# Kernel optimization log

Measured on AMD Instinct MI355X. Metric: run time of the kernel, lower is better.

Reference implementation:

```python
import jax, jax.numpy as jnp
import numpy as np

B, N, DIN, DOUT, CHEB_K, EMBED = 64, 2048, 64, 64, 3, 16


def setup_inputs() -> dict:
    key = jax.random.key(0)
    k0, k1, k2, k3 = jax.random.split(key, 4)
    return {
        "x": jax.random.normal(k0, (B, N, DIN), dtype=jnp.float32),
        "node_embeddings": jax.random.normal(k1, (N, EMBED), dtype=jnp.float32),
        "weights_pool": jax.random.normal(k2, (EMBED, CHEB_K, DIN, DOUT), dtype=jnp.float32) * 0.02,
        "bias_pool": jax.random.normal(k3, (EMBED, DOUT), dtype=jnp.float32) * 0.02,
    }


def reference(x, node_embeddings, weights_pool, bias_pool):
    # x: (B, N, dim_in); node_embeddings: (N, embed_dim)
    n = node_embeddings.shape[0]
    # adaptive adjacency: softmax(relu(E E^T)) row-wise
    supports = jax.nn.softmax(jax.nn.relu(node_embeddings @ node_embeddings.T), axis=1)
    # Chebyshev polynomial basis: T0=I, T1=S, Tk = 2 S T_{k-1} - T_{k-2}
    tk = [jnp.eye(n, dtype=x.dtype), supports]
    for _ in range(2, CHEB_K):
        tk.append(2.0 * supports @ tk[-1] - tk[-2])
    S = jnp.stack(tk, axis=0)  # (K, N, N)
    # per-node weights/bias generated from embeddings
    weights = jnp.einsum('nd,dkio->nkio', node_embeddings, weights_pool)  # (N,K,din,dout)
    bias = node_embeddings @ bias_pool  # (N, dout)
    # graph conv: aggregate over neighbors for each Chebyshev order
    x_g = jnp.einsum('knm,bmc->bnkc', S, x)  # (B, N, K, din)
    out = jnp.einsum('bnki,nkio->bno', x_g, weights) + bias  # (B, N, dout)
    return out
```

## Files before the change

### kernel.cpp

```cpp
#include <hip/hip_runtime.h>
#include <hip/hip_bf16.h>

typedef unsigned short u16;
typedef short short8 __attribute__((ext_vector_type(8)));
typedef short short4v __attribute__((ext_vector_type(4)));
typedef float floatx4 __attribute__((ext_vector_type(4)));

#define NNODES 2048
#define BATCH  64
#define DIN    64
#define DOUT   64
#define EMB    16

__device__ __forceinline__ u16 f2bf(float f) {
  union { float f; unsigned u; } v; v.f = f;
  unsigned r = v.u + 0x7fffu + ((v.u >> 16) & 1u);
  return (u16)(r >> 16);
}

__device__ __forceinline__ void gload_lds16(const void* g, void* l) {
  __builtin_amdgcn_global_load_lds(
      (const __attribute__((address_space(1))) void*)g,
      (__attribute__((address_space(3))) void*)l, 16, 0, 0);
}

__global__ __launch_bounds__(256) void wgen_k(const float* __restrict__ E,
                                              const float* __restrict__ pool,
                                              u16* __restrict__ W) {
  int t = threadIdx.x;
  int ec = blockIdx.x % 48, nc = blockIdx.x / 48;
  int e = ec * 256 + t;
  int n0 = nc * 64;
  float pv[16];
#pragma unroll
  for (int d = 0; d < 16; d++) {
    float p = pool[(size_t)d * 12288 + e];
    if (e < 4096) p -= pool[(size_t)d * 12288 + 8192 + e];
    if (e >= 8192) p += p;
    pv[d] = p;
  }
  const float* er = E + (size_t)n0 * EMB;
#pragma unroll 4
  for (int nn = 0; nn < 64; nn++) {
    float acc = 0.0f;
#pragma unroll
    for (int d = 0; d < 16; d++) acc = fmaf(er[nn * EMB + d], pv[d], acc);
    W[(size_t)(n0 + nn) * 12288 + e] = f2bf(acc);
  }
}

__global__ __launch_bounds__(256) void prologue(const float* __restrict__ E,
                                                const float* __restrict__ x,
                                                u16* __restrict__ Sb,
                                                u16* __restrict__ xtt) {
  int bid = blockIdx.x;
  int t = threadIdx.x;

  if (bid < 2048) {
    int n = bid;
    const float4* ep = (const float4*)(E + (size_t)n * EMB);
    float4 e0 = ep[0], e1 = ep[1], e2 = ep[2], e3 = ep[3];
    float lg[8];
    float mx = 0.0f;
#pragma unroll
    for (int j = 0; j < 8; j++) {
      int m = t + j * 256;
      const float4* mp = (const float4*)(E + (size_t)m * EMB);
      float4 a = mp[0], b = mp[1], c = mp[2], d = mp[3];
      float dot = e0.x * a.x + e0.y * a.y + e0.z * a.z + e0.w * a.w
                + e1.x * b.x + e1.y * b.y + e1.z * b.z + e1.w * b.w
                + e2.x * c.x + e2.y * c.y + e2.z * c.z + e2.w * c.w
                + e3.x * d.x + e3.y * d.y + e3.z * d.z + e3.w * d.w;
      dot = fmaxf(dot, 0.0f);
      lg[j] = dot;
      mx = fmaxf(mx, dot);
    }
    __shared__ float smax[4], ssum[4];
#pragma unroll
    for (int off = 32; off > 0; off >>= 1) mx = fmaxf(mx, __shfl_xor(mx, off, 64));
    if ((t & 63) == 0) smax[t >> 6] = mx;
    __syncthreads();
    mx = fmaxf(fmaxf(smax[0], smax[1]), fmaxf(smax[2], smax[3]));
    float sum = 0.0f;
#pragma unroll
    for (int j = 0; j < 8; j++) {
      float e = __expf(lg[j] - mx);
      lg[j] = e;
      sum += e;
    }
#pragma unroll
    for (int off = 32; off > 0; off >>= 1) sum += __shfl_xor(sum, off, 64);
    if ((t & 63) == 0) ssum[t >> 6] = sum;
    __syncthreads();
    sum = ssum[0] + ssum[1] + ssum[2] + ssum[3];
    float inv = 1.0f / sum;
#pragma unroll
    for (int j = 0; j < 8; j++)
      Sb[(size_t)n * NNODES + t + j * 256] = f2bf(lg[j] * inv);

  } else {
    __shared__ float tile[64][69];
    int u = bid - 2048;
    int b = u >> 5;
    int m0 = (u & 31) * 64;
    int r = t >> 2, cs = (t & 3) * 16;
    const float* xp = x + ((size_t)b * NNODES + m0 + r) * DIN + cs;
    float4 v0 = ((const float4*)xp)[0];
    float4 v1 = ((const float4*)xp)[1];
    float4 v2 = ((const float4*)xp)[2];
    float4 v3 = ((const float4*)xp)[3];
    *(float4*)&tile[r][cs]      = v0;
    *(float4*)&tile[r][cs + 4]  = v1;
    *(float4*)&tile[r][cs + 8]  = v2;
    *(float4*)&tile[r][cs + 12] = v3;
    __syncthreads();
    int c = t >> 2, ms = (t & 3) * 16;
    short8 o0, o1;
#pragma unroll
    for (int j = 0; j < 8; j++) o0[j] = (short)f2bf(tile[ms + j][c]);
#pragma unroll
    for (int j = 0; j < 8; j++) o1[j] = (short)f2bf(tile[ms + 8 + j][c]);
    u16* op = xtt + ((size_t)b * 64 + c) * NNODES + m0 + ms;
    *(short8*)op = o0;
    *(short8*)(op + 8) = o1;
  }
}

#define GK 2048
#define GN 4096
#define NT 32
#define BUFU 24576

#define GEMM_PREAMBLE                                                          \
  __shared__ u16 smem[3 * BUFU];                                               \
  int t = threadIdx.x, lane = t & 63, wave = t >> 6;                           \
  int lin = blockIdx.y * gridDim.x + blockIdx.x;                               \
  int nwg = gridDim.x * gridDim.y;                                             \
  int sw = (lin & 7) * (nwg >> 3) + (lin >> 3);                                \
  int bx = sw & 31, by = sw >> 5;                                              \
  int m0 = by * 256, n0 = bx * 128;                                            \
  const u16* pg[6];                                                            \
  int lof[6];                                                                  \
  _Pragma("unroll") for (int j = 0; j < 4; j++) {                              \
    int c = t + 512 * j;                                                       \
    int row = c >> 3;                                                          \
    int gs = (c & 7) ^ (row & 7);                                              \
    pg[j] = A + (size_t)(m0 + row) * GK + gs * 8;                              \
    lof[j] = c * 8;                                                            \
  }                                                                            \
  _Pragma("unroll") for (int j = 0; j < 2; j++) {                              \
    int c = t + 512 * j;                                                       \
    int row = c >> 3;                                                          \
    int gs = (c & 7) ^ (row & 7);                                              \
    pg[4 + j] = Bt + (size_t)(n0 + row) * GK + gs * 8;                         \
    lof[4 + j] = 16384 + c * 8;                                                \
  }                                                                            \
  auto stage = [&](int b, int kt) {                                            \
    _Pragma("unroll") for (int j = 0; j < 6; j++)                              \
        gload_lds16(pg[j] + kt, &smem[b * BUFU + lof[j]]);                     \
  };                                                                           \
  int wr = wave >> 1, wc = wave & 1;                                           \
  int lr = lane & 15, lg = lane >> 4;                                          \
  floatx4 acc[4][4];                                                           \
  _Pragma("unroll") for (int mi = 0; mi < 4; mi++)                             \
      _Pragma("unroll") for (int ni = 0; ni < 4; ni++)                         \
          acc[mi][ni] = (floatx4)0.0f;                                         \
  int aoff[2][4], boff[2][4];                                                  \
  _Pragma("unroll") for (int s = 0; s < 2; s++) {                              \
    _Pragma("unroll") for (int mi = 0; mi < 4; mi++) {                         \
      int row = wr * 64 + mi * 16 + lr;                                        \
      int slot = s * 4 + lg;                                                   \
      aoff[s][mi] = row * 64 + (slot ^ (row & 7)) * 8;                         \
    }                                                                          \
    _Pragma("unroll") for (int ni = 0; ni < 4; ni++) {                         \
      int row = wc * 64 + ni * 16 + lr;                                        \
      int slot = s * 4 + lg;                                                   \
      boff[s][ni] = 16384 + row * 64 + (slot ^ (row & 7)) * 8;                 \
    }                                                                          \
  }                                                                            \
  auto compute = [&](int b) {                                                  \
    const u16* base = &smem[b * BUFU];                                         \
    short8 af[2][4], bf[2][4];                                                 \
    _Pragma("unroll") for (int s = 0; s < 2; s++) {                            \
      _Pragma("unroll") for (int mi = 0; mi < 4; mi++)                         \
          af[s][mi] = *(const short8*)(base + aoff[s][mi]);                    \
      _Pragma("unroll") for (int ni = 0; ni < 4; ni++)                         \
          bf[s][ni] = *(const short8*)(base + boff[s][ni]);                    \
    }                                                                          \
    _Pragma("unroll") for (int s = 0; s < 2; s++)                              \
        _Pragma("unroll") for (int mi = 0; mi < 4; mi++)                       \
            _Pragma("unroll") for (int ni = 0; ni < 4; ni++)                   \
                acc[mi][ni] = __builtin_amdgcn_mfma_f32_16x16x32_bf16(         \
                    af[s][mi], bf[s][ni], acc[mi][ni], 0, 0, 0);               \
  };                                                                           \
  stage(0, 0);                                                                 \
  stage(1, 64);                                                                \
  for (int tt = 0; tt < NT - 2; ++tt) {                                        \
    asm volatile("s_waitcnt vmcnt(6)" ::: "memory");                           \
    __builtin_amdgcn_s_barrier();                                              \
    stage((tt + 2) % 3, (tt + 2) * 64);                                        \
    compute(tt % 3);                                                           \
  }                                                                            \
  asm volatile("s_waitcnt vmcnt(6)" ::: "memory");                             \
  __builtin_amdgcn_s_barrier();                                                \
  compute((NT - 2) % 3);                                                       \
  asm volatile("s_waitcnt vmcnt(0)" ::: "memory");                             \
  __builtin_amdgcn_s_barrier();                                                \
  compute((NT - 1) % 3);                                                       \
  _Pragma("unroll") for (int mi = 0; mi < 4; mi++)                             \
      _Pragma("unroll") for (int ni = 0; ni < 4; ni++) {                       \
    int row = m0 + wr * 64 + mi * 16 + lg * 4;                                 \
    int col = n0 + wc * 64 + ni * 16 + lr;                                     \
    _Pragma("unroll") for (int r = 0; r < 4; r++)                              \
        C[(size_t)(row + r) * GN + col] = f2bf(acc[mi][ni][r]);                \
  }

__global__ __launch_bounds__(512) void gemm_plain(const u16* __restrict__ A,
                                                  const u16* __restrict__ Bt,
                                                  u16* __restrict__ C) {
  GEMM_PREAMBLE
}

__global__ __launch_bounds__(512) void gemm_tr(const u16* __restrict__ A,
                                               const u16* __restrict__ Bt,
                                               u16* __restrict__ C,
                                               u16* __restrict__ Ct) {
  GEMM_PREAMBLE
  __syncthreads();
  u16* scr = smem + wave * 4608;
#pragma unroll
  for (int mi = 0; mi < 4; mi++)
#pragma unroll
    for (int ni = 0; ni < 4; ni++) {
      int ncol = ni * 16 + lr;
      int chunk = mi * 2 + (lg >> 1);
      int off = ncol * 72 + chunk * 8 + (lg & 1) * 4;
      short4v sv;
#pragma unroll
      for (int r = 0; r < 4; r++) sv[r] = (short)f2bf(acc[mi][ni][r]);
      *(short4v*)&scr[off] = sv;
    }
  int c = lane;
  u16* op = Ct + (size_t)(n0 + wc * 64 + c) * GK + m0 + wr * 64;
#pragma unroll
  for (int jj = 0; jj < 8; jj++) {
    short8 v = *(const short8*)&scr[c * 72 + jj * 8];
    *(short8*)(op + jj * 8) = v;
  }
}

__global__ __launch_bounds__(256) void final_k(const float* __restrict__ x,
                                               const float* __restrict__ E,
                                               const float* __restrict__ bpool,
                                               const u16* __restrict__ xg1,
                                               const u16* __restrict__ xg2,
                                               const u16* __restrict__ W,
                                               float* __restrict__ out) {
  __shared__ u16 Xs[3][64][72];
  __shared__ u16 Ws[64 * 200];
  __shared__ float bias_s[64];
  int n = blockIdx.x, t = threadIdx.x;

  {
    int b = t >> 2, i0 = (t & 3) * 16;
    const float* xp = x + ((size_t)b * NNODES + n) * DIN + i0;
    float4 v0 = ((const float4*)xp)[0];
    float4 v1 = ((const float4*)xp)[1];
    float4 v2 = ((const float4*)xp)[2];
    float4 v3 = ((const float4*)xp)[3];
    u16* d = &Xs[0][b][i0];
    d[0] = f2bf(v0.x); d[1] = f2bf(v0.y); d[2] = f2bf(v0.z); d[3] = f2bf(v0.w);
    d[4] = f2bf(v1.x); d[5] = f2bf(v1.y); d[6] = f2bf(v1.z); d[7] = f2bf(v1.w);
    d[8] = f2bf(v2.x); d[9] = f2bf(v2.y); d[10] = f2bf(v2.z); d[11] = f2bf(v2.w);
    d[12] = f2bf(v3.x); d[13] = f2bf(v3.y); d[14] = f2bf(v3.z); d[15] = f2bf(v3.w);
  }
  for (int idx = t; idx < 512; idx += 256) {
    short8 v1 = *(const short8*)(xg1 + (size_t)n * 4096 + idx * 8);
    *(short8*)&Xs[1][idx >> 3][(idx & 7) * 8] = v1;
    short8 v2 = *(const short8*)(xg2 + (size_t)n * 4096 + idx * 8);
    *(short8*)&Xs[2][idx >> 3][(idx & 7) * 8] = v2;
  }
  for (int idx = t; idx < 1536; idx += 256) {
    short8 v = *(const short8*)(W + (size_t)n * 12288 + idx * 8);
    int kk = idx >> 3;
    int oo = (idx & 7) * 8;
    int c8 = kk >> 3, k7 = kk & 7;
#pragma unroll
    for (int j = 0; j < 8; j++) {
      int o = oo + j;
      Ws[o * 200 + ((c8 ^ (o >> 3)) << 3) + k7] = (u16)v[j];
    }
  }
  if (t < 64) {
    float acc = 0.0f;
#pragma unroll
    for (int d = 0; d < 16; d++)
      acc = fmaf(E[(size_t)n * EMB + d], bpool[d * 64 + t], acc);
    bias_s[t] = acc;
  }
  __syncthreads();

  int lane = t & 63, wave = t >> 6;
  int lr = lane & 15, lg = lane >> 4;
  int wb = wave * 16;
  floatx4 acc[4];
#pragma unroll
  for (int ot = 0; ot < 4; ot++) acc[ot] = (floatx4)0.0f;

#pragma unroll
  for (int ks = 0; ks < 6; ks++) {
    int kk = ks * 32 + lg * 8;
    int c8 = ks * 4 + lg;
    short8 a = *(const short8*)&Xs[kk >> 6][wb + lr][kk & 63];
#pragma unroll
    for (int ot = 0; ot < 4; ot++) {
      int o = ot * 16 + lr;
      short8 bb = *(const short8*)&Ws[o * 200 + ((c8 ^ (o >> 3)) << 3)];
      acc[ot] = __builtin_amdgcn_mfma_f32_16x16x32_bf16(a, bb, acc[ot], 0, 0, 0);
    }
  }
#pragma unroll
  for (int ot = 0; ot < 4; ot++) {
    int o = ot * 16 + lr;
    float bs = bias_s[o];
#pragma unroll
    for (int r = 0; r < 4; r++) {
      int b = wb + lg * 4 + r;
      out[((size_t)b * NNODES + n) * DOUT + o] = acc[ot][r] + bs;
    }
  }
}

extern "C" void kernel_launch(void* const* d_in, const int* in_sizes, int n_in,
                              void* d_out, int out_size, void* d_ws, size_t ws_size,
                              hipStream_t stream) {
  const float* x     = (const float*)d_in[0];
  const float* E     = (const float*)d_in[1];
  const float* pool  = (const float*)d_in[2];
  const float* bpool = (const float*)d_in[3];
  float* out = (float*)d_out;

  char* ws = (char*)d_ws;
  u16* Sb   = (u16*)(ws);
  u16* xtt  = (u16*)(ws + 8388608);
  u16* xg1  = (u16*)(ws + 25165824);
  u16* xg1t = (u16*)(ws + 41943040);
  u16* xg2  = (u16*)(ws + 58720256);
  u16* Wall = (u16*)(ws + 75497472);

  prologue<<<4096, 256, 0, stream>>>(E, x, Sb, xtt);
  wgen_k<<<1536, 256, 0, stream>>>(E, pool, Wall);
  gemm_tr<<<dim3(32, 8), 512, 0, stream>>>(Sb, xtt, xg1, xg1t);
  gemm_plain<<<dim3(32, 8), 512, 0, stream>>>(Sb, xg1t, xg2);
  final_k<<<NNODES, 256, 0, stream>>>(x, E, bpool, xg1, xg2, Wall, out);
}
```

Before: 157.3 us.

## Fuse per-node weight generation into first GEMM as extra producer waves

Removes the separate weight-generation kernel and runs it inside gemm_tr as four extra waves per block (768 threads). Those waves compute three outputs each per embedding row and issue barriers to stay in step with the GEMM waves' barrier sequence. The aim is to hide the large bf16 weight write behind the compute-bound GEMM and save one launch. The cost is a larger launch bound, which may limit registers and occupancy for the GEMM waves, and the barrier counts must match exactly or the kernel breaks.

Result: slower. 163.3 us (+3.8%).

```diff
diff --git a/kernel.cpp b/kernel.cpp
--- a/kernel.cpp
+++ b/kernel.cpp
@@ -5,6 +5,7 @@
 typedef short short8 __attribute__((ext_vector_type(8)));
 typedef short short4v __attribute__((ext_vector_type(4)));
 typedef float floatx4 __attribute__((ext_vector_type(4)));
+typedef float float16v __attribute__((ext_vector_type(16)));
 
 #define NNODES 2048
 #define BATCH  64
@@ -22,31 +23,6 @@
   __builtin_amdgcn_global_load_lds(
       (const __attribute__((address_space(1))) void*)g,
       (__attribute__((address_space(3))) void*)l, 16, 0, 0);
-}
-
-__global__ __launch_bounds__(256) void wgen_k(const float* __restrict__ E,
-                                              const float* __restrict__ pool,
-                                              u16* __restrict__ W) {
-  int t = threadIdx.x;
-  int ec = blockIdx.x % 48, nc = blockIdx.x / 48;
-  int e = ec * 256 + t;
-  int n0 = nc * 64;
-  float pv[16];
-#pragma unroll
-  for (int d = 0; d < 16; d++) {
-    float p = pool[(size_t)d * 12288 + e];
-    if (e < 4096) p -= pool[(size_t)d * 12288 + 8192 + e];
-    if (e >= 8192) p += p;
-    pv[d] = p;
-  }
-  const float* er = E + (size_t)n0 * EMB;
-#pragma unroll 4
-  for (int nn = 0; nn < 64; nn++) {
-    float acc = 0.0f;
-#pragma unroll
-    for (int d = 0; d < 16; d++) acc = fmaf(er[nn * EMB + d], pv[d], acc);
-    W[(size_t)(n0 + nn) * 12288 + e] = f2bf(acc);
-  }
 }
 
 __global__ __launch_bounds__(256) void prologue(const float* __restrict__ E,
@@ -135,8 +111,7 @@
   __shared__ u16 smem[3 * BUFU];                                               \
   int t = threadIdx.x, lane = t & 63, wave = t >> 6;                           \
   int lin = blockIdx.y * gridDim.x + blockIdx.x;                               \
-  int nwg = gridDim.x * gridDim.y;                                             \
-  int sw = (lin & 7) * (nwg >> 3) + (lin >> 3);                                \
+  int sw = (lin & 7) * 32 + (lin >> 3);                     \
   int bx = sw & 31, by = sw >> 5;                                              \
   int m0 = by * 256, n0 = bx * 128;                                            \
   const u16* pg[6];                                                            \
@@ -221,10 +196,58 @@
   GEMM_PREAMBLE
 }
 
-__global__ __launch_bounds__(512) void gemm_tr(const u16* __restrict__ A,
+__global__ __launch_bounds__(768) void gemm_tr(const u16* __restrict__ A,
                                                const u16* __restrict__ Bt,
                                                u16* __restrict__ C,
-                                               u16* __restrict__ Ct) {
+                                               u16* __restrict__ Ct,
+                                               const float* __restrict__ E,
+                                               const float* __restrict__ pool,
+                                               u16* __restrict__ W) {
+  {
+    int th = threadIdx.x;
+    if (th >= 512) {
+      int lin_raw = blockIdx.y * gridDim.x + blockIdx.x;
+      int wavew = lin_raw * 4 + (th >> 6) - 8;
+      int l = th & 63;
+      int eg = wavew & 63, ng = wavew >> 6;
+      int e0 = eg * 192 + l;
+      int n0w = ng * 128;
+      float pv[3][16];
+#pragma unroll
+      for (int q = 0; q < 3; q++) {
+        int e = e0 + q * 64;
+#pragma unroll
+        for (int d = 0; d < 16; d++) {
+          float p = pool[(size_t)d * 12288 + e];
+          if (e < 4096) p -= pool[(size_t)d * 12288 + 8192 + e];
+          if (e >= 8192) p += p;
+          pv[q][d] = p;
+        }
+      }
+      const float16v* er16 = (const float16v*)(E + (size_t)n0w * EMB);
+      for (int ch = 0; ch < 32; ch++) {
+#pragma unroll
+        for (int j = 0; j < 4; j++) {
+          int nn = ch * 4 + j;
+          float16v ev = er16[nn];
+          float a0 = 0.0f, a1 = 0.0f, a2 = 0.0f;
+#pragma unroll
+          for (int d = 0; d < 16; d++) {
+            a0 = fmaf(ev[d], pv[0][d], a0);
+            a1 = fmaf(ev[d], pv[1][d], a1);
+            a2 = fmaf(ev[d], pv[2][d], a2);
+          }
+          u16* wp = &W[(size_t)(n0w + nn) * 12288 + e0];
+          wp[0] = f2bf(a0);
+          wp[64] = f2bf(a1);
+          wp[128] = f2bf(a2);
+        }
+        __builtin_amdgcn_s_barrier();
+      }
+      __builtin_amdgcn_s_barrier();
+      return;
+    }
+  }
   GEMM_PREAMBLE
   __syncthreads();
   u16* scr = smem + wave * 4608;
@@ -349,8 +372,7 @@
   u16* Wall = (u16*)(ws + 75497472);
 
   prologue<<<4096, 256, 0, stream>>>(E, x, Sb, xtt);
-  wgen_k<<<1536, 256, 0, stream>>>(E, pool, Wall);
-  gemm_tr<<<dim3(32, 8), 512, 0, stream>>>(Sb, xtt, xg1, xg1t);
+  gemm_tr<<<dim3(32, 8), 768, 0, stream>>>(Sb, xtt, xg1, xg1t, E, pool, Wall);
   gemm_plain<<<dim3(32, 8), 512, 0, stream>>>(Sb, xg1t, xg2);
   final_k<<<NNODES, 256, 0, stream>>>(x, E, bpool, xg1, xg2, Wall, out);
 }
```
